# Performance work log

Hardware: AMD Instinct MI355X
Metric: run time of the kernel (lower is better)

Reference implementation:

```python
import jax, jax.numpy as jnp
import numpy as np

B, Q, P, HID = 1, 1024, 1024, 4096
NH, NKV, D = 32, 4, 128
MAXPOS = 2048
N_REP = NH // NKV


def rotate_half(x):
    x1, x2 = jnp.split(x, 2, axis=-1)
    return jnp.concatenate((-x2, x1), axis=-1)


def setup_inputs() -> dict:
    key = jax.random.key(0)
    ks = jax.random.split(key, 8)
    hidden_states = jax.random.normal(ks[0], (B, Q, HID), jnp.float32) * 0.02
    past_key_value = jax.random.normal(ks[1], (B, 2, NKV, P, D), jnp.float32)
    # additive causal mask buffer covering [B, NH, MAXPOS, MAXPOS]
    tril = jnp.tril(jnp.ones((MAXPOS, MAXPOS), jnp.bool_))
    mask2d = jnp.where(tril, 0.0, -1e9).astype(jnp.float32)
    attention_mask = jnp.broadcast_to(mask2d[None, None], (B, NH, MAXPOS, MAXPOS))
    Wq = jax.random.normal(ks[2], (HID, HID), jnp.float32) * 0.02
    Wk = jax.random.normal(ks[3], (NKV * D, HID), jnp.float32) * 0.02
    Wv = jax.random.normal(ks[4], (NKV * D, HID), jnp.float32) * 0.02
    Wo = jax.random.normal(ks[5], (HID, HID), jnp.float32) * 0.02
    return {"hidden_states": hidden_states, "past_key_value": past_key_value,
            "attention_mask": attention_mask, "Wq": Wq, "Wk": Wk, "Wv": Wv, "Wo": Wo}


def reference(hidden_states, past_key_value, attention_mask, Wq, Wk, Wv, Wo):
    kv_len = P + Q
    # projections (torch Linear: y = x @ W^T)
    q = jnp.einsum('bqh,oh->bqo', hidden_states, Wq).reshape(B, Q, NH, D).transpose(0, 2, 1, 3)
    k = jnp.einsum('bqh,oh->bqo', hidden_states, Wk).reshape(B, Q, NKV, D).transpose(0, 2, 1, 3)
    v = jnp.einsum('bqh,oh->bqo', hidden_states, Wv).reshape(B, Q, NKV, D).transpose(0, 2, 1, 3)
    # append to KV cache BEFORE RoPE (faithful to source ordering)
    past_k = past_key_value[:, 0]  # [B, NKV, P, D]
    past_v = past_key_value[:, 1]
    k = jnp.concatenate((past_k, k), axis=2)  # [B, NKV, kv_len, D]
    v = jnp.concatenate((past_v, v), axis=2)
    new_past = jnp.stack((k, v), axis=1)
    # rotary embedding: keys use positions [0, kv_len), queries [P, kv_len)
    inv_freq = 1.0 / (10000.0 ** (jnp.arange(0, D, 2, dtype=jnp.float32) / D))
    t = jnp.arange(kv_len, dtype=jnp.float32)
    freqs = jnp.einsum('i,j->ij', t, inv_freq)
    emb = jnp.concatenate((freqs, freqs), axis=-1)  # [kv_len, D]
    cos = jnp.cos(emb)[None, None]  # [1,1,kv_len,D]
    sin = jnp.sin(emb)[None, None]
    q = q * cos[:, :, P:kv_len] + rotate_half(q) * sin[:, :, P:kv_len]
    k = k * cos + rotate_half(k) * sin
    # causal mask slice: rows [kv_len-Q, kv_len), cols [0, kv_len)
    causal_mask = attention_mask[:, :, P:kv_len, :kv_len]
    # GQA broadcast of KV heads
    k = jnp.repeat(k, N_REP, axis=1)  # [B, NH, kv_len, D]
    v = jnp.repeat(v, N_REP, axis=1)
    scores = jnp.einsum('bhqd,bhkd->bhqk', q, k) / np.sqrt(D).astype(np.float32)
    scores = scores + causal_mask
    probs = jax.nn.softmax(scores, axis=-1)
    ctx = jnp.einsum('bhqk,bhkd->bhqd', probs, v)  # [B, NH, Q, D]
    ctx = ctx.transpose(0, 2, 1, 3).reshape(B, Q, HID)
    attn_output = jnp.einsum('bqh,oh->bqo', ctx, Wo)
    return attn_output, new_past
```

## Files before the change

kernel.cpp:

```cpp
#include <hip/hip_runtime.h>
#include <cstdint>
#include <cstddef>

typedef __attribute__((ext_vector_type(4))) float f32x4;
typedef __attribute__((ext_vector_type(8))) unsigned short u16x8;
typedef __attribute__((ext_vector_type(4))) unsigned short u16x4;
typedef __bf16 bf16x8 __attribute__((ext_vector_type(8)));

__device__ __forceinline__ unsigned short f2bf(float f) {
  unsigned u = __builtin_bit_cast(unsigned, f);
  u += 0x7FFF + ((u >> 16) & 1);
  return (unsigned short)(u >> 16);
}

__device__ __forceinline__ float bf2f(unsigned short u) {
  unsigned x = (unsigned)u << 16;
  return __builtin_bit_cast(float, x);
}

__device__ __forceinline__ void mfma16x16x32(f32x4& acc, u16x8 a, u16x8 b) {
  acc = __builtin_amdgcn_mfma_f32_16x16x32_bf16(
      __builtin_bit_cast(bf16x8, a), __builtin_bit_cast(bf16x8, b), acc, 0, 0, 0);
}

typedef __attribute__((address_space(1))) const unsigned int as1_u32;
typedef __attribute__((address_space(3))) unsigned int as3_u32;
__device__ __forceinline__ void load_lds16(const void* g, void* l) {
  __builtin_amdgcn_global_load_lds((as1_u32*)g, (as3_u32*)l, 16, 0, 0);
}

#define QSCALE2 0.12751745f

__global__ void k_cvt_all(const float* __restrict__ hs, const float* __restrict__ wq,
                          const float* __restrict__ wk, const float* __restrict__ wv,
                          const float* __restrict__ wo,
                          unsigned short* __restrict__ hs_bf, unsigned short* __restrict__ w_bf,
                          float2* __restrict__ tab) {
  const int total = 10616832;
  int stride = gridDim.x * blockDim.x;
  for (int i = blockIdx.x * blockDim.x + threadIdx.x; i < total; i += stride) {
    if (i >= 10485760) {
      int j = i - 10485760;
      int t = j >> 6, f = j & 63;
      float inv = expf(-(float)f * 0.14391156831212787f);
      float ang = (float)t * inv;
      tab[j] = make_float2(cosf(ang), sinf(ang));
      continue;
    }
    const float4* src;
    unsigned short* dst;
    long j;
    if (i < 1048576) { src = (const float4*)hs; j = i; dst = hs_bf + (size_t)i * 4; }
    else {
      int t = i - 1048576;
      dst = w_bf + (size_t)t * 4;
      if (t < 4194304)      { src = (const float4*)wq; j = t; }
      else if (t < 4718592) { src = (const float4*)wk; j = t - 4194304; }
      else if (t < 5242880) { src = (const float4*)wv; j = t - 4718592; }
      else                  { src = (const float4*)wo; j = t - 5242880; }
    }
    float4 v = src[j];
    u16x4 o = { f2bf(v.x), f2bf(v.y), f2bf(v.z), f2bf(v.w) };
    *(u16x4*)dst = o;
  }
}

__global__ __launch_bounds__(256) void k_gemm_bt(
    const unsigned short* __restrict__ A, const unsigned short* __restrict__ Bt,
    unsigned short* __restrict__ C, int M, int N, int K, int KC) {
  __shared__ unsigned short lA[2][128 * 32];
  __shared__ unsigned short lB[2][128 * 32];
  const int tid = threadIdx.x;
  const int w = tid >> 6, lane = tid & 63;
  const int wm = w >> 1, wn = w & 1;
  const int m0 = blockIdx.y * 128, n0 = blockIdx.x * 128;
  const int k0 = blockIdx.z * KC;
  const int lr = lane & 15, lg = lane >> 4;
  unsigned short* Cp = C + (size_t)blockIdx.z * M * N;

  f32x4 acc[4][4];
#pragma unroll
  for (int i = 0; i < 4; i++)
#pragma unroll
    for (int j = 0; j < 4; j++) acc[i][j] = (f32x4){0.f, 0.f, 0.f, 0.f};

  const int srow = w * 32 + (lane >> 2);
  const int scol = (lane & 3) * 8;
  const unsigned short* gA = A + (size_t)(m0 + srow) * K + scol;
  const unsigned short* gB = Bt + (size_t)(n0 + srow) * K + scol;

  auto stage = [&](int buf, int kt) {
#pragma unroll
    for (int c = 0; c < 2; c++) {
      load_lds16(gA + (size_t)c * 16 * K + kt, &lA[buf][(w * 32 + c * 16) * 32]);
      load_lds16(gB + (size_t)c * 16 * K + kt, &lB[buf][(w * 32 + c * 16) * 32]);
    }
  };

  stage(0, k0);
  __syncthreads();
  int cur = 0;
  for (int kt = k0; kt < k0 + KC; kt += 32) {
    if (kt + 32 < k0 + KC) stage(cur ^ 1, kt + 32);
    u16x8 af[4], bf[4];
#pragma unroll
    for (int i = 0; i < 4; i++) af[i] = *(const u16x8*)&lA[cur][(wm * 64 + i * 16 + lr) * 32 + lg * 8];
#pragma unroll
    for (int j = 0; j < 4; j++) bf[j] = *(const u16x8*)&lB[cur][(wn * 64 + j * 16 + lr) * 32 + lg * 8];
#pragma unroll
    for (int i = 0; i < 4; i++)
#pragma unroll
      for (int j = 0; j < 4; j++) mfma16x16x32(acc[i][j], af[i], bf[j]);
    __syncthreads();
    cur ^= 1;
  }
#pragma unroll
  for (int i = 0; i < 4; i++)
#pragma unroll
    for (int j = 0; j < 4; j++)
#pragma unroll
      for (int r = 0; r < 4; r++) {
        int row = m0 + wm * 64 + i * 16 + lg * 4 + r;
        int col = n0 + wn * 64 + j * 16 + lr;
        Cp[(size_t)row * N + col] = f2bf(acc[i][j][r]);
      }
}

__global__ void k_reduce4(const u16x4* __restrict__ p, float4* __restrict__ out,
                          int n4, size_t stride4) {
  int stridet = gridDim.x * blockDim.x;
  for (int i = blockIdx.x * blockDim.x + threadIdx.x; i < n4; i += stridet) {
    u16x4 a = p[i], b = p[i + stride4], c = p[i + 2 * stride4], d = p[i + 3 * stride4];
    out[i] = make_float4((bf2f(a[0]) + bf2f(b[0])) + (bf2f(c[0]) + bf2f(d[0])),
                         (bf2f(a[1]) + bf2f(b[1])) + (bf2f(c[1]) + bf2f(d[1])),
                         (bf2f(a[2]) + bf2f(b[2])) + (bf2f(c[2]) + bf2f(d[2])),
                         (bf2f(a[3]) + bf2f(b[3])) + (bf2f(c[3]) + bf2f(d[3])));
  }
}

#define GP_S 5242880
__device__ __forceinline__ float gsum(const unsigned short* __restrict__ gp, size_t i) {
  return (bf2f(gp[i]) + bf2f(gp[i + GP_S])) +
         (bf2f(gp[i + 2 * (size_t)GP_S]) + bf2f(gp[i + 3 * (size_t)GP_S]));
}

__global__ void k_post(const float* __restrict__ past, const unsigned short* __restrict__ gp,
                       float* __restrict__ outk, float* __restrict__ outv,
                       unsigned short* __restrict__ kr, unsigned short* __restrict__ vt,
                       unsigned short* __restrict__ qr, const float2* __restrict__ tab) {
  int idx = blockIdx.x * blockDim.x + threadIdx.x;
  if (idx < 524288) {
    int d0 = idx & 63;
    int t = (idx >> 6) & 2047;
    int h = idx >> 17;
    float v1, v2;
    if (t < 1024) {
      const float* p = past + ((size_t)h * 1024 + t) * 128;
      v1 = p[d0]; v2 = p[d0 + 64];
    } else {
      size_t base = (size_t)(t - 1024) * 5120 + 4096 + h * 128;
      v1 = gsum(gp, base + d0); v2 = gsum(gp, base + d0 + 64);
    }
    float* o = outk + ((size_t)h * 2048 + t) * 128;
    o[d0] = v1; o[d0 + 64] = v2;
    float2 cs = tab[t * 64 + d0];
    unsigned short* ko = kr + ((size_t)h * 2048 + t) * 128;
    ko[d0]      = f2bf(v1 * cs.x - v2 * cs.y);
    ko[d0 + 64] = f2bf(v2 * cs.x + v1 * cs.y);
  } else if (idx < 1572864) {
    int i = idx - 524288;
    int d = i & 127;
    int t = (i >> 7) & 2047;
    int h = i >> 18;
    float val = (t < 1024) ? past[4 * 1024 * 128 + ((size_t)h * 1024 + t) * 128 + d]
                           : gsum(gp, (size_t)(t - 1024) * 5120 + 4608 + h * 128 + d);
    outv[((size_t)h * 2048 + t) * 128 + d] = val;
    vt[((size_t)h * 128 + d) * 2048 + t] = f2bf(val);
  } else {
    int i = idx - 1572864;
    int d0 = i & 63;
    int q = (i >> 6) & 1023;
    int h = i >> 16;
    size_t base = (size_t)q * 5120 + h * 128;
    float v1 = gsum(gp, base + d0), v2 = gsum(gp, base + d0 + 64);
    float2 cs = tab[(1024 + q) * 64 + d0];
    unsigned short* o = qr + ((size_t)h * 1024 + q) * 128;
    o[d0]      = f2bf((v1 * cs.x - v2 * cs.y) * QSCALE2);
    o[d0 + 64] = f2bf((v2 * cs.x + v1 * cs.y) * QSCALE2);
  }
}

__global__ __launch_bounds__(512) void k_attn8(
    const unsigned short* __restrict__ qr,
    const unsigned short* __restrict__ kr,
    const unsigned short* __restrict__ vt,
    unsigned short* __restrict__ ctxb) {
  __shared__ unsigned short k_lds[2][64 * 128];
  __shared__ unsigned short v_lds[2][128 * 64];
  __shared__ unsigned short plds[8][640];
  const int bid = blockIdx.x;
  const int h = bid >> 3;
  const int c = bid & 7;
  const int kvh = h >> 3;
  const int tid = threadIdx.x;
  const int w = tid >> 6, l = tid & 63;
  const int lr = l & 15, lg = l >> 4;
  const int q0 = c * 128 + w * 16;
  const unsigned short* kh = kr + (size_t)kvh * 2048 * 128;
  const unsigned short* vh = vt + (size_t)kvh * 128 * 2048;

  u16x8 qf[4];
  {
    const unsigned short* qb = qr + ((size_t)(h * 1024 + q0 + lr)) * 128 + lg * 8;
#pragma unroll
    for (int ks = 0; ks < 4; ks++) qf[ks] = *(const u16x8*)(qb + ks * 32);
  }
  f32x4 acc[8];
#pragma unroll
  for (int i = 0; i < 8; i++) acc[i] = (f32x4){0.f, 0.f, 0.f, 0.f};
  float m_r = -1e30f, l_r = 0.f;

  const int limit = 1024 + q0 + lr;
  const int mylimit = 1024 + q0 + 15;
  const int T = 18 + 2 * c;

  auto stageK = [&](int buf, int kb) {
#pragma unroll
    for (int i = 0; i < 2; i++) {
      int loff = i * 8192 + tid * 16;
      int row = loff >> 8;
      int scb = (loff & 255) ^ ((row & 7) << 4);
      load_lds16((const char*)(kh + (size_t)(kb + row) * 128) + scb,
                 (char*)&k_lds[buf][0] + loff);
    }
  };
  auto stageV = [&](int buf, int kb) {
#pragma unroll
    for (int i = 0; i < 2; i++) {
      int loff = i * 8192 + tid * 16;
      int row = loff >> 7;
      int scb = (loff & 127) ^ ((row & 7) << 4);
      load_lds16((const char*)(vh + (size_t)row * 2048 + kb) + scb,
                 (char*)&v_lds[buf][0] + loff);
    }
  };

  stageK(0, 0); stageV(0, 0);
  __syncthreads();
  int cur = 0;
  for (int t = 0; t < T; t++) {
    if (t + 1 < T) { stageK(cur ^ 1, (t + 1) * 64); stageV(cur ^ 1, (t + 1) * 64); }
    if (t * 64 <= mylimit) {
#pragma unroll
      for (int kc = 0; kc < 2; kc++) {
        const int kb = t * 64 + kc * 32;
        if (kb > mylimit) continue;
        f32x4 s[2];
#pragma unroll
        for (int sub = 0; sub < 2; sub++) {
          f32x4 a = (f32x4){0.f, 0.f, 0.f, 0.f};
          const int key = kc * 32 + sub * 16 + lr;
          const int swz = (key & 7) << 4;
#pragma unroll
          for (int ks = 0; ks < 4; ks++) {
            int addr = key * 256 + ((ks * 64 + lg * 16) ^ swz);
            u16x8 kf = *(const u16x8*)((const char*)&k_lds[cur][0] + addr);
            mfma16x16x32(a, kf, qf[ks]);
          }
          s[sub] = a;
        }
        float v[8];
#pragma unroll
        for (int r = 0; r < 4; r++) { v[r] = s[0][r]; v[4 + r] = s[1][r]; }
        if (kb + 31 > 1024 + q0) {
          const int kbase = kb + lg * 4;
#pragma unroll
          for (int r = 0; r < 4; r++) {
            if (kbase + r > limit)      v[r]     = -1e30f;
            if (kbase + 16 + r > limit) v[4 + r] = -1e30f;
          }
        }
        float tmax = v[0];
#pragma unroll
        for (int j = 1; j < 8; j++) tmax = fmaxf(tmax, v[j]);
        tmax = fmaxf(tmax, __shfl_xor(tmax, 16));
        tmax = fmaxf(tmax, __shfl_xor(tmax, 32));
        if (!__all(tmax <= m_r + 11.5f)) {
          float mn = fmaxf(m_r, tmax);
          float corr = exp2f(m_r - mn);
          m_r = mn;
          l_r *= corr;
#pragma unroll
          for (int nt = 0; nt < 8; nt++)
#pragma unroll
            for (int r = 0; r < 4; r++) acc[nt][r] *= corr;
        }
        float p[8];
        float psum = 0.f;
#pragma unroll
        for (int j = 0; j < 8; j++) { p[j] = exp2f(v[j] - m_r); psum += p[j]; }
        psum += __shfl_xor(psum, 16);
        psum += __shfl_xor(psum, 32);
        l_r += psum;
        unsigned wds[4];
#pragma unroll
        for (int j = 0; j < 4; j++) {
          unsigned lo = __builtin_bit_cast(unsigned, p[2 * j]) + 0x8000u;
          unsigned hi = __builtin_bit_cast(unsigned, p[2 * j + 1]) + 0x8000u;
          wds[j] = (hi & 0xFFFF0000u) | (lo >> 16);
        }
        char* pb = (char*)&plds[w][0] + lr * 80 + lg * 8;
        *(uint2*)(pb)      = make_uint2(wds[0], wds[1]);
        *(uint2*)(pb + 32) = make_uint2(wds[2], wds[3]);
        asm volatile("s_waitcnt lgkmcnt(0)" ::: "memory");
        u16x8 pf = *(const u16x8*)&plds[w][lr * 40 + lg * 8];
#pragma unroll
        for (int nt = 0; nt < 8; nt++) {
          const int d = nt * 16 + lr;
          int addr = d * 128 + ((kc * 64 + lg * 16) ^ ((d & 7) << 4));
          u16x8 vf = *(const u16x8*)((const char*)&v_lds[cur][0] + addr);
          mfma16x16x32(acc[nt], vf, pf);
        }
      }
    }
    __syncthreads();
    cur ^= 1;
  }
  float inv = 1.0f / l_r;
  unsigned short* ob = ctxb + (size_t)(q0 + lr) * 4096 + h * 128 + lg * 4;
#pragma unroll
  for (int nt = 0; nt < 8; nt++) {
    u16x4 o = { f2bf(acc[nt][0] * inv), f2bf(acc[nt][1] * inv),
                f2bf(acc[nt][2] * inv), f2bf(acc[nt][3] * inv) };
    *(u16x4*)(ob + nt * 16) = o;
  }
}

extern "C" void kernel_launch(void* const* d_in, const int* in_sizes, int n_in,
                              void* d_out, int out_size, void* d_ws, size_t ws_size,
                              hipStream_t stream) {
  (void)in_sizes; (void)n_in; (void)out_size; (void)ws_size;
  const float* hs   = (const float*)d_in[0];
  const float* past = (const float*)d_in[1];
  const float* Wq = (const float*)d_in[3];
  const float* Wk = (const float*)d_in[4];
  const float* Wv = (const float*)d_in[5];
  const float* Wo = (const float*)d_in[6];

  float* out_attn = (float*)d_out;
  float* out_pk = out_attn + 4194304;
  float* out_pv = out_pk + 1048576;

  const size_t MB = 1048576;
  char* ws = (char*)d_ws;
  unsigned short* hs_bf   = (unsigned short*)(ws);
  unsigned short* wqkv_bf = (unsigned short*)(ws + 8 * MB);
  unsigned short* wo_bf   = (unsigned short*)(ws + 48 * MB);
  float2*         tab     = (float2*)(ws + 100 * MB);
  unsigned short* kr      = (unsigned short*)(ws + 101 * MB);
  unsigned short* vt      = (unsigned short*)(ws + 103 * MB);
  unsigned short* qr      = (unsigned short*)(ws + 105 * MB);
  unsigned short* ctxb    = (unsigned short*)(ws + 113 * MB);
  unsigned short* gp      = (unsigned short*)(ws + 128 * MB);

  k_cvt_all<<<2048, 256, 0, stream>>>(hs, Wq, Wk, Wv, Wo, hs_bf, wqkv_bf, tab);

  dim3 g1(5120 / 128, 1024 / 128, 4);
  k_gemm_bt<<<g1, 256, 0, stream>>>(hs_bf, wqkv_bf, gp, 1024, 5120, 4096, 1024);

  k_post<<<14336, 256, 0, stream>>>(past, gp, out_pk, out_pv, kr, vt, qr, tab);

  k_attn8<<<256, 512, 0, stream>>>(qr, kr, vt, ctxb);

  dim3 g2(4096 / 128, 1024 / 128, 4);
  k_gemm_bt<<<g2, 256, 0, stream>>>(ctxb, wo_bf, gp, 1024, 4096, 4096, 1024);
  k_reduce4<<<2048, 256, 0, stream>>>((const u16x4*)gp, (float4*)out_attn,
                                      1048576, 1048576);
}
```

Before: 256.4 us.

## Fuse split-K reductions into GEMMs via last-arriving-block atomic counters

After: 731.8 us. +185.4%, slower.

```diff
diff --git a/kernel.cpp b/kernel.cpp
--- a/kernel.cpp
+++ b/kernel.cpp
@@ -30,6 +30,12 @@
 }
 
 #define QSCALE2 0.12751745f
+#define GP_S 5242880
+
+__device__ __forceinline__ float gsum(const unsigned short* __restrict__ gp, size_t i) {
+  return (bf2f(gp[i]) + bf2f(gp[i + GP_S])) +
+         (bf2f(gp[i + 2 * (size_t)GP_S]) + bf2f(gp[i + 3 * (size_t)GP_S]));
+}
 
 __global__ void k_cvt_all(const float* __restrict__ hs, const float* __restrict__ wq,
                           const float* __restrict__ wk, const float* __restrict__ wv,
@@ -65,9 +71,14 @@
   }
 }
 
-__global__ __launch_bounds__(256) void k_gemm_bt(
+__global__ __launch_bounds__(256, 3) void k_gemm1_post(
     const unsigned short* __restrict__ A, const unsigned short* __restrict__ Bt,
-    unsigned short* __restrict__ C, int M, int N, int K, int KC) {
+    unsigned short* __restrict__ gp,
+    const float* __restrict__ past, const float2* __restrict__ tab,
+    float* __restrict__ outk, float* __restrict__ outv,
+    unsigned short* __restrict__ kr, unsigned short* __restrict__ vt,
+    unsigned short* __restrict__ qr, unsigned int* __restrict__ cnt) {
+  const int M = 1024, N = 5120, K = 4096, KC = 1024;
   __shared__ unsigned short lA[2][128 * 32];
   __shared__ unsigned short lB[2][128 * 32];
   const int tid = threadIdx.x;
@@ -76,7 +87,7 @@
   const int m0 = blockIdx.y * 128, n0 = blockIdx.x * 128;
   const int k0 = blockIdx.z * KC;
   const int lr = lane & 15, lg = lane >> 4;
-  unsigned short* Cp = C + (size_t)blockIdx.z * M * N;
+  unsigned short* Cp = gp + (size_t)blockIdx.z * M * N;
 
   f32x4 acc[4][4];
 #pragma unroll
@@ -124,69 +135,74 @@
         int col = n0 + wn * 64 + j * 16 + lr;
         Cp[(size_t)row * N + col] = f2bf(acc[i][j][r]);
       }
-}
-
-__global__ void k_reduce4(const u16x4* __restrict__ p, float4* __restrict__ out,
-                          int n4, size_t stride4) {
-  int stridet = gridDim.x * blockDim.x;
-  for (int i = blockIdx.x * blockDim.x + threadIdx.x; i < n4; i += stridet) {
-    u16x4 a = p[i], b = p[i + stride4], c = p[i + 2 * stride4], d = p[i + 3 * stride4];
-    out[i] = make_float4((bf2f(a[0]) + bf2f(b[0])) + (bf2f(c[0]) + bf2f(d[0])),
-                         (bf2f(a[1]) + bf2f(b[1])) + (bf2f(c[1]) + bf2f(d[1])),
-                         (bf2f(a[2]) + bf2f(b[2])) + (bf2f(c[2]) + bf2f(d[2])),
-                         (bf2f(a[3]) + bf2f(b[3])) + (bf2f(c[3]) + bf2f(d[3])));
-  }
-}
-
-#define GP_S 5242880
-__device__ __forceinline__ float gsum(const unsigned short* __restrict__ gp, size_t i) {
-  return (bf2f(gp[i]) + bf2f(gp[i + GP_S])) +
-         (bf2f(gp[i + 2 * (size_t)GP_S]) + bf2f(gp[i + 3 * (size_t)GP_S]));
-}
-
-__global__ void k_post(const float* __restrict__ past, const unsigned short* __restrict__ gp,
-                       float* __restrict__ outk, float* __restrict__ outv,
-                       unsigned short* __restrict__ kr, unsigned short* __restrict__ vt,
-                       unsigned short* __restrict__ qr, const float2* __restrict__ tab) {
-  int idx = blockIdx.x * blockDim.x + threadIdx.x;
-  if (idx < 524288) {
-    int d0 = idx & 63;
-    int t = (idx >> 6) & 2047;
-    int h = idx >> 17;
-    float v1, v2;
-    if (t < 1024) {
-      const float* p = past + ((size_t)h * 1024 + t) * 128;
-      v1 = p[d0]; v2 = p[d0 + 64];
-    } else {
-      size_t base = (size_t)(t - 1024) * 5120 + 4096 + h * 128;
-      v1 = gsum(gp, base + d0); v2 = gsum(gp, base + d0 + 64);
-    }
-    float* o = outk + ((size_t)h * 2048 + t) * 128;
-    o[d0] = v1; o[d0 + 64] = v2;
-    float2 cs = tab[t * 64 + d0];
-    unsigned short* ko = kr + ((size_t)h * 2048 + t) * 128;
-    ko[d0]      = f2bf(v1 * cs.x - v2 * cs.y);
-    ko[d0 + 64] = f2bf(v2 * cs.x + v1 * cs.y);
-  } else if (idx < 1572864) {
-    int i = idx - 524288;
-    int d = i & 127;
-    int t = (i >> 7) & 2047;
-    int h = i >> 18;
-    float val = (t < 1024) ? past[4 * 1024 * 128 + ((size_t)h * 1024 + t) * 128 + d]
-                           : gsum(gp, (size_t)(t - 1024) * 5120 + 4608 + h * 128 + d);
-    outv[((size_t)h * 2048 + t) * 128 + d] = val;
-    vt[((size_t)h * 128 + d) * 2048 + t] = f2bf(val);
+
+  __threadfence();
+  __syncthreads();
+  __shared__ unsigned int sflag;
+  if (tid == 0) sflag = atomicAdd(&cnt[blockIdx.y * gridDim.x + blockIdx.x], 1u);
+  __syncthreads();
+  if (sflag != 3u) return;
+  __threadfence();
+
+  if (n0 < 4096) {
+    const int h = n0 >> 7;
+    for (int pass = 0; pass < 32; ++pass) {
+      int flat = pass * 256 + tid;
+      int d0 = flat & 63, row = flat >> 6;
+      int q = m0 + row;
+      size_t base = (size_t)q * 5120 + n0;
+      float v1 = gsum(gp, base + d0), v2 = gsum(gp, base + d0 + 64);
+      float2 cs = tab[(1024 + q) * 64 + d0];
+      unsigned short* o = qr + ((size_t)h * 1024 + q) * 128;
+      o[d0]      = f2bf((v1 * cs.x - v2 * cs.y) * QSCALE2);
+      o[d0 + 64] = f2bf((v2 * cs.x + v1 * cs.y) * QSCALE2);
+    }
+  } else if (n0 < 4608) {
+    const int h = (n0 - 4096) >> 7;
+    for (int pass = 0; pass < 32; ++pass) {
+      int flat = pass * 256 + tid;
+      int d0 = flat & 63, row = flat >> 6;
+      {
+        int t = 1024 + m0 + row;
+        size_t base = (size_t)(m0 + row) * 5120 + n0;
+        float v1 = gsum(gp, base + d0), v2 = gsum(gp, base + d0 + 64);
+        float* o = outk + ((size_t)h * 2048 + t) * 128;
+        o[d0] = v1; o[d0 + 64] = v2;
+        float2 cs = tab[t * 64 + d0];
+        unsigned short* ko = kr + ((size_t)h * 2048 + t) * 128;
+        ko[d0]      = f2bf(v1 * cs.x - v2 * cs.y);
+        ko[d0 + 64] = f2bf(v2 * cs.x + v1 * cs.y);
+      }
+      {
+        int t = m0 + row;
+        const float* p = past + ((size_t)h * 1024 + t) * 128;
+        float v1 = p[d0], v2 = p[d0 + 64];
+        float* o = outk + ((size_t)h * 2048 + t) * 128;
+        o[d0] = v1; o[d0 + 64] = v2;
+        float2 cs = tab[t * 64 + d0];
+        unsigned short* ko = kr + ((size_t)h * 2048 + t) * 128;
+        ko[d0]      = f2bf(v1 * cs.x - v2 * cs.y);
+        ko[d0 + 64] = f2bf(v2 * cs.x + v1 * cs.y);
+      }
+    }
   } else {
-    int i = idx - 1572864;
-    int d0 = i & 63;
-    int q = (i >> 6) & 1023;
-    int h = i >> 16;
-    size_t base = (size_t)q * 5120 + h * 128;
-    float v1 = gsum(gp, base + d0), v2 = gsum(gp, base + d0 + 64);
-    float2 cs = tab[(1024 + q) * 64 + d0];
-    unsigned short* o = qr + ((size_t)h * 1024 + q) * 128;
-    o[d0]      = f2bf((v1 * cs.x - v2 * cs.y) * QSCALE2);
-    o[d0 + 64] = f2bf((v2 * cs.x + v1 * cs.y) * QSCALE2);
+    const int h = (n0 - 4608) >> 7;
+    for (int pass = 0; pass < 64; ++pass) {
+      int flat = pass * 256 + tid;
+      int d = flat & 127, row = flat >> 7;
+      {
+        int t = 1024 + m0 + row;
+        float val = gsum(gp, (size_t)(m0 + row) * 5120 + n0 + d);
+        outv[((size_t)h * 2048 + t) * 128 + d] = val;
+        vt[((size_t)h * 128 + d) * 2048 + t] = f2bf(val);
+      }
+      {
+        int t = m0 + row;
+        float val = past[524288 + ((size_t)h * 1024 + t) * 128 + d];
+        outv[((size_t)h * 2048 + t) * 128 + d] = val;
+        vt[((size_t)h * 128 + d) * 2048 + t] = f2bf(val);
+      }
+    }
   }
 }
 
@@ -336,6 +352,91 @@
   }
 }
 
+__global__ __launch_bounds__(256, 3) void k_gemm2_red(
+    const unsigned short* __restrict__ A, const unsigned short* __restrict__ Bt,
+    unsigned short* __restrict__ gp2, float* __restrict__ out_attn,
+    unsigned int* __restrict__ cnt) {
+  const int M = 1024, N = 4096, K = 4096, KC = 1024;
+  __shared__ unsigned short lA[2][128 * 32];
+  __shared__ unsigned short lB[2][128 * 32];
+  const int tid = threadIdx.x;
+  const int w = tid >> 6, lane = tid & 63;
+  const int wm = w >> 1, wn = w & 1;
+  const int m0 = blockIdx.y * 128, n0 = blockIdx.x * 128;
+  const int k0 = blockIdx.z * KC;
+  const int lr = lane & 15, lg = lane >> 4;
+  unsigned short* Cp = gp2 + (size_t)blockIdx.z * M * N;
+
+  f32x4 acc[4][4];
+#pragma unroll
+  for (int i = 0; i < 4; i++)
+#pragma unroll
+    for (int j = 0; j < 4; j++) acc[i][j] = (f32x4){0.f, 0.f, 0.f, 0.f};
+
+  const int srow = w * 32 + (lane >> 2);
+  const int scol = (lane & 3) * 8;
+  const unsigned short* gA = A + (size_t)(m0 + srow) * K + scol;
+  const unsigned short* gB = Bt + (size_t)(n0 + srow) * K + scol;
+
+  auto stage = [&](int buf, int kt) {
+#pragma unroll
+    for (int c = 0; c < 2; c++) {
+      load_lds16(gA + (size_t)c * 16 * K + kt, &lA[buf][(w * 32 + c * 16) * 32]);
+      load_lds16(gB + (size_t)c * 16 * K + kt, &lB[buf][(w * 32 + c * 16) * 32]);
+    }
+  };
+
+  stage(0, k0);
+  __syncthreads();
+  int cur = 0;
+  for (int kt = k0; kt < k0 + KC; kt += 32) {
+    if (kt + 32 < k0 + KC) stage(cur ^ 1, kt + 32);
+    u16x8 af[4], bf[4];
+#pragma unroll
+    for (int i = 0; i < 4; i++) af[i] = *(const u16x8*)&lA[cur][(wm * 64 + i * 16 + lr) * 32 + lg * 8];
+#pragma unroll
+    for (int j = 0; j < 4; j++) bf[j] = *(const u16x8*)&lB[cur][(wn * 64 + j * 16 + lr) * 32 + lg * 8];
+#pragma unroll
+    for (int i = 0; i < 4; i++)
+#pragma unroll
+      for (int j = 0; j < 4; j++) mfma16x16x32(acc[i][j], af[i], bf[j]);
+    __syncthreads();
+    cur ^= 1;
+  }
+#pragma unroll
+  for (int i = 0; i < 4; i++)
+#pragma unroll
+    for (int j = 0; j < 4; j++)
+#pragma unroll
+      for (int r = 0; r < 4; r++) {
+        int row = m0 + wm * 64 + i * 16 + lg * 4 + r;
+        int col = n0 + wn * 64 + j * 16 + lr;
+        Cp[(size_t)row * N + col] = f2bf(acc[i][j][r]);
+      }
+
+  __threadfence();
+  __syncthreads();
+  __shared__ unsigned int sflag;
+  if (tid == 0) sflag = atomicAdd(&cnt[blockIdx.y * gridDim.x + blockIdx.x], 1u);
+  __syncthreads();
+  if (sflag != 3u) return;
+  __threadfence();
+
+  const size_t S = (size_t)M * N;
+  for (int pass = 0; pass < 16; ++pass) {
+    int flat = pass * 256 + tid;
+    int row = flat >> 5, c4 = flat & 31;
+    size_t idx = (size_t)(m0 + row) * 4096 + n0 + c4 * 4;
+    const unsigned short* g = gp2 + idx;
+    float4 o;
+    o.x = (bf2f(g[0]) + bf2f(g[S])) + (bf2f(g[2 * S]) + bf2f(g[3 * S]));
+    o.y = (bf2f(g[1]) + bf2f(g[1 + S])) + (bf2f(g[1 + 2 * S]) + bf2f(g[1 + 3 * S]));
+    o.z = (bf2f(g[2]) + bf2f(g[2 + S])) + (bf2f(g[2 + 2 * S]) + bf2f(g[2 + 3 * S]));
+    o.w = (bf2f(g[3]) + bf2f(g[3 + S])) + (bf2f(g[3 + 2 * S]) + bf2f(g[3 + 3 * S]));
+    *(float4*)(out_attn + idx) = o;
+  }
+}
+
 extern "C" void kernel_launch(void* const* d_in, const int* in_sizes, int n_in,
                               void* d_out, int out_size, void* d_ws, size_t ws_size,
                               hipStream_t stream) {
@@ -356,6 +457,8 @@
   unsigned short* hs_bf   = (unsigned short*)(ws);
   unsigned short* wqkv_bf = (unsigned short*)(ws + 8 * MB);
   unsigned short* wo_bf   = (unsigned short*)(ws + 48 * MB);
+  unsigned int*   cnt1    = (unsigned int*)(ws + 99 * MB);
+  unsigned int*   cnt2    = cnt1 + 512;
   float2*         tab     = (float2*)(ws + 100 * MB);
   unsigned short* kr      = (unsigned short*)(ws + 101 * MB);
   unsigned short* vt      = (unsigned short*)(ws + 103 * MB);
@@ -363,17 +466,16 @@
   unsigned short* ctxb    = (unsigned short*)(ws + 113 * MB);
   unsigned short* gp      = (unsigned short*)(ws + 128 * MB);
 
+  hipMemsetAsync(cnt1, 0, 8192, stream);
+
   k_cvt_all<<<2048, 256, 0, stream>>>(hs, Wq, Wk, Wv, Wo, hs_bf, wqkv_bf, tab);
 
   dim3 g1(5120 / 128, 1024 / 128, 4);
-  k_gemm_bt<<<g1, 256, 0, stream>>>(hs_bf, wqkv_bf, gp, 1024, 5120, 4096, 1024);
-
-  k_post<<<14336, 256, 0, stream>>>(past, gp, out_pk, out_pv, kr, vt, qr, tab);
+  k_gemm1_post<<<g1, 256, 0, stream>>>(hs_bf, wqkv_bf, gp, past, tab,
+                                       out_pk, out_pv, kr, vt, qr, cnt1);
 
   k_attn8<<<256, 512, 0, stream>>>(qr, kr, vt, ctxb);
 
   dim3 g2(4096 / 128, 1024 / 128, 4);
-  k_gemm_bt<<<g2, 256, 0, stream>>>(ctxb, wo_bf, gp, 1024, 4096, 4096, 1024);
-  k_reduce4<<<2048, 256, 0, stream>>>((const u16x4*)gp, (float4*)out_attn,
-                                      1048576, 1048576);
-}
+  k_gemm2_red<<<g2, 256, 0, stream>>>(ctxb, wo_bf, gp, out_attn, cnt2);
+}
```
